# Kernel optimization log

Hardware: AMD Instinct MI355X
Metric: run time of the kernel (lower is better)

The kernel has to match this reference:

```python
import jax, jax.numpy as jnp
import numpy as np


def setup_inputs() -> dict:
    key = jax.random.key(0)
    ks = jax.random.split(key, 5)
    B, C, H, W = 32, 2048, 14, 14
    K = 113  # num_concepts + 1
    NUM_CLASSES = 200
    x = jax.random.normal(ks[0], (B, C, H, W), dtype=jnp.float32)
    concepts = jax.random.normal(ks[1], (K, C), dtype=jnp.float32)
    # small init scale for linear heads (keeps sigmoid/logits in a sane range)
    concept_fc_w = jax.random.normal(ks[2], (1, C), dtype=jnp.float32) * 0.02
    concept_fc_b = jnp.zeros((1,), dtype=jnp.float32)
    label_fc_w = jax.random.normal(ks[3], (NUM_CLASSES, C), dtype=jnp.float32) * 0.02
    label_fc_b = jnp.zeros((NUM_CLASSES,), dtype=jnp.float32)
    return {
        "x": x,
        "concepts": concepts,
        "concept_fc_w": concept_fc_w,
        "concept_fc_b": concept_fc_b,
        "label_fc_w": label_fc_w,
        "label_fc_b": label_fc_b,
    }


def reference(x, concepts, concept_fc_w, concept_fc_b, label_fc_w, label_fc_b):
    b, c, h, w = x.shape
    h2, w2 = h * 2, w * 2
    # F.interpolate(mode='bilinear', align_corners=False) == jax.image.resize bilinear
    x = jax.image.resize(x, (b, c, h2, w2), method="bilinear")
    xe = x.reshape(b, c, h2 * w2).transpose(0, 2, 1)  # [b, n, c]
    # cdist(concepts, xe, p=2) via matmul expansion (matches torch's mm-based cdist)
    x_sq = jnp.sum(xe * xe, axis=-1)                    # [b, n]
    c_sq = jnp.sum(concepts * concepts, axis=-1)        # [k]
    dots = jnp.einsum("kc,bnc->bkn", concepts, xe)      # [b, k, n]
    d2 = c_sq[None, :, None] + x_sq[:, None, :] - 2.0 * dots
    dists = jnp.sqrt(jnp.maximum(d2, 0.0))              # [b, k, n]
    attn = jax.nn.softmax(-dists, axis=1)               # softmax over concepts
    score_maps = attn.reshape(b, -1, h2, w2)            # [b, k, h2, w2]
    concept_vecs = jnp.einsum("bkn,bnc->bkc", attn[:, :-1, :], xe)  # [b, k-1, c]
    logits = jnp.einsum("bkc,c->bk", concept_vecs, concept_fc_w[0]) + concept_fc_b[0]
    concept_scores = jax.nn.sigmoid(logits)             # [b, k-1]
    preds = (concept_scores @ concepts[:-1, :]) @ label_fc_w.T + label_fc_b  # [b, 200]
    return score_maps, concept_scores, preds
```

## Files before the change

kernel.cpp:

```cpp
#include <hip/hip_runtime.h>
#include <hip/hip_bf16.h>
#include <cstdint>

typedef __attribute__((ext_vector_type(8))) short short8;
typedef __attribute__((ext_vector_type(4))) float f32x4;
typedef __attribute__((ext_vector_type(16))) float f32x16;

#define BDIM 32
#define CDIM 2048
#define NPIX 196
#define HIN 14
#define N2 784
#define W2 28
#define KDIM 113
#define KC 112
#define NCLS 200
#define NBX 14
#define BNC 56
#define NSTEP 64
#define PST 224
#define GST 200
#define RDST 68
#define SSTB 60

__global__ __launch_bounds__(256) void k_prep(const float* __restrict__ concepts,
                                              const float* __restrict__ cfcw,
                                              ushort* __restrict__ cbf,
                                              float* __restrict__ csq) {
  int k = blockIdx.x, t = threadIdx.x;
  const int kt = k >> 5, row = k & 31;
  float s = 0.f;
  for (int c = t; c < CDIM; c += 256) {
    float v = (k < KDIM) ? concepts[(size_t)k * CDIM + c] : (k == KDIM ? cfcw[c] : 0.f);
    __hip_bfloat16 h = __float2bfloat16(v);
    int st = c >> 5, it = (c >> 4) & 1, g2 = (c >> 3) & 1, j = c & 7;
    cbf[(((size_t)st * 4 + kt) * 2 + it) * 512 + (g2 * 32 + row) * 8 + j] = __bfloat16_as_ushort(h);
    float vb = __bfloat162float(h);
    s = fmaf(vb, vb, s);
  }
  __shared__ float r[4];
#pragma unroll
  for (int off = 32; off > 0; off >>= 1) s += __shfl_down(s, off, 64);
  if ((t & 63) == 0) r[t >> 6] = s;
  __syncthreads();
  if (t == 0) csq[k] = r[0] + r[1] + r[2] + r[3];
}

__global__ __launch_bounds__(512, 2) void k_xt(const float* __restrict__ x,
                                               ushort* __restrict__ xt,
                                               float* __restrict__ Gpart) {
  __shared__ float P[32 * PST];
  __shared__ float Gw[8][16][65];
  const int sg = blockIdx.x, b = blockIdx.y;
  const int tid = threadIdx.x;
  const int lane = tid & 63, wv = tid >> 6;
  const int chg = tid >> 4, seg = tid & 15;
  const int p0 = seg * 13;

  for (int z = tid; z < 32 * 28; z += 512) {
    int c = z / 28, j = z - c * 28;
    P[c * PST + 196 + j] = 0.f;
  }

  float g[13][5];
#pragma unroll
  for (int p = 0; p < 13; ++p)
#pragma unroll
    for (int t = 0; t < 5; ++t) g[p][t] = 0.f;

  for (int si = 0; si < 4; ++si) {
    const int s = sg * 4 + si;
    __syncthreads();
    {
      const float4* src = (const float4*)(x + ((size_t)b * CDIM + s * 32) * NPIX);
#pragma unroll
      for (int i = 0; i < 3; ++i) {
        int q = tid + i * 512;
        int c = q / 49, pq = q - c * 49;
        *(float4*)&P[c * PST + 4 * pq] = src[q];
      }
      if (tid < 32) {
        int q = 1536 + tid;
        int c = q / 49, pq = q - c * 49;
        *(float4*)&P[c * PST + 4 * pq] = src[q];
      }
    }
    __syncthreads();
#pragma unroll
    for (int pass = 0; pass < 2; ++pass) {
      int slot = tid + pass * 512;
      if (slot < 896) {
        int t = slot >> 7, r = slot & 127;
        int it = r >> 6, l = r & 63;
        int pxp = t * 32 + (l & 31);
        int row = pxp >> 4, col = pxp & 15;
        int c0 = it * 16 + (l >> 5) * 8;
        uint uu[4];
        if (col < 14) {
          int px = row * HIN + col;
#pragma unroll
          for (int p = 0; p < 4; ++p) {
            float v0 = P[(c0 + 2 * p) * PST + px];
            float v1 = P[(c0 + 2 * p + 1) * PST + px];
            uu[p] = (uint)__bfloat16_as_ushort(__float2bfloat16(v0)) |
                    ((uint)__bfloat16_as_ushort(__float2bfloat16(v1)) << 16);
          }
        } else {
          uu[0] = uu[1] = uu[2] = uu[3] = 0u;
        }
        uint4 pk; pk.x = uu[0]; pk.y = uu[1]; pk.z = uu[2]; pk.w = uu[3];
        *(uint4*)&xt[((((size_t)b * 7 + t) * 64 + s) * 1024) + it * 512 + (size_t)l * 8] = pk;
      }
    }
    {
      float xv[28];
      const float* Pr = &P[chg * PST];
#pragma unroll
      for (int i = 0; i < 7; ++i) *(float4*)&xv[4 * i] = *(const float4*)&Pr[p0 + 4 * i];
#pragma unroll
      for (int p = 0; p < 13; ++p) {
        float a = xv[p];
        g[p][0] = fmaf(a, a, g[p][0]);
        g[p][1] = fmaf(a, xv[p + 1], g[p][1]);
        g[p][2] = fmaf(a, xv[p + 13], g[p][2]);
        g[p][3] = fmaf(a, xv[p + 14], g[p][3]);
        g[p][4] = fmaf(a, xv[p + 15], g[p][4]);
      }
    }
  }
#pragma unroll
  for (int p = 0; p < 13; ++p)
#pragma unroll
    for (int t = 0; t < 5; ++t) {
      float v = g[p][t];
      v += __shfl_xor(v, 16, 64);
      v += __shfl_xor(v, 32, 64);
      g[p][t] = v;
    }
  if (lane < 16) {
#pragma unroll
    for (int p = 0; p < 13; ++p)
#pragma unroll
      for (int t = 0; t < 5; ++t) Gw[wv][lane][p * 5 + t] = g[p][t];
  }
  __syncthreads();
#pragma unroll
  for (int it = 0; it < 2; ++it) {
    int slot = tid + it * 512;
    if (slot < 16 * 65) {
      int sseg = slot / 65, i = slot - sseg * 65;
      float v = 0.f;
#pragma unroll
      for (int ww = 0; ww < 8; ++ww) v += Gw[ww][sseg][i];
      int pl = i / 5, ty = i - pl * 5;
      int px = sseg * 13 + pl;
      if (px < NPIX)
        Gpart[((size_t)b * 16 + sg) * (5 * GST) + ty * GST + px] = v;
    }
  }
}

__global__ __launch_bounds__(256) void k_gred(const float* __restrict__ Gpart,
                                              float* __restrict__ Gs) {
  const int b = blockIdx.x, tid = threadIdx.x;
  for (int i = tid; i < 5 * GST; i += 256) {
    float v = 0.f;
#pragma unroll
    for (int sg = 0; sg < 16; ++sg) v += Gpart[((size_t)b * 16 + sg) * (5 * GST) + i];
    Gs[(size_t)b * (5 * GST) + i] = v;
  }
}

__global__ __launch_bounds__(256, 3) void k_gemm3(
    const ushort* __restrict__ xt,
    const ushort* __restrict__ cbf,
    const float* __restrict__ Gs,
    const float* __restrict__ csq,
    float* __restrict__ attn_out,
    float* __restrict__ part)
{
  __shared__ float RDs[128 * RDST];
  __shared__ ushort Ssb[KDIM * SSTB];
  __shared__ float csq_s[KDIM];
  __shared__ float xsqs[BNC], projs2[BNC];

  const int tid = threadIdx.x;
  const int wgid = blockIdx.x;
  const int xcd = wgid & 7, slot = wgid >> 3;
  const int bq = slot / NBX, bx = slot - bq * NBX;
  const int b = xcd + 8 * bq;
  const int n0 = bx * BNC;
  const int lane = tid & 63, w = tid >> 6;

  int r0 = bx - 1; if (r0 < 0) r0 = 0; if (r0 > 11) r0 = 11;
  const int T0 = r0 >> 1;

  if (tid < KDIM) csq_s[tid] = csq[tid];

  const ushort* abp = cbf + w * 1024 + lane * 8;
  const ushort* xtb = xt + (((size_t)b * 7 + T0) << 16) + lane * 8;

  f32x16 acc[2];
#pragma unroll
  for (int tt = 0; tt < 2; ++tt)
#pragma unroll
    for (int r = 0; r < 16; ++r) acc[tt][r] = 0.f;

#define LOADSET(A_, B_, S_)                                              \
  do {                                                                   \
    const size_t so_ = (size_t)(S_) * 4096;                              \
    const size_t xo_ = (size_t)(S_) * 1024;                              \
    A_[0] = *(const uint4*)(abp + so_);                                  \
    A_[1] = *(const uint4*)(abp + so_ + 512);                            \
    B_[0][0] = *(const uint4*)(xtb + xo_);                               \
    B_[0][1] = *(const uint4*)(xtb + xo_ + 512);                         \
    B_[1][0] = *(const uint4*)(xtb + 65536 + xo_);                       \
    B_[1][1] = *(const uint4*)(xtb + 65536 + xo_ + 512);                 \
  } while (0)

#define COMPUTE(A_, B_)                                                  \
  do {                                                                   \
    _Pragma("unroll")                                                    \
    for (int it_ = 0; it_ < 2; ++it_) {                                  \
      short8 af_ = *(const short8*)&A_[it_];                             \
      acc[0] = __builtin_amdgcn_mfma_f32_32x32x16_bf16(                  \
          af_, *(const short8*)&B_[0][it_], acc[0], 0, 0, 0);            \
      acc[1] = __builtin_amdgcn_mfma_f32_32x32x16_bf16(                  \
          af_, *(const short8*)&B_[1][it_], acc[1], 0, 0, 0);            \
    }                                                                    \
  } while (0)

  uint4 a0[2], a1[2], b0[2][2], b1[2][2];
  LOADSET(a0, b0, 0);
  for (int s = 0; s < NSTEP; s += 2) {
    if (s + 1 < NSTEP) LOADSET(a1, b1, s + 1);
    COMPUTE(a0, b0);
    if (s + 2 < NSTEP) LOADSET(a0, b0, s + 2);
    COMPUTE(a1, b1);
  }
#undef LOADSET
#undef COMPUTE

#pragma unroll
  for (int tt = 0; tt < 2; ++tt)
#pragma unroll
    for (int r = 0; r < 16; ++r) {
      int row = w * 32 + (r & 3) + 8 * (r >> 2) + 4 * (lane >> 5);
      RDs[row * RDST + tt * 32 + (lane & 31)] = acc[tt][r];
    }
  __syncthreads();

  auto COLW = [&](int col, int& p1, int& p3, int& p1g, int& p3g,
                  float& w00, float& w01, float& w10, float& w11) {
    const int i2 = 2 * bx + (col >= 28 ? 1 : 0);
    const int j2 = col - (col >= 28 ? 28 : 0);
    float si = 0.5f * i2 - 0.25f, sj = 0.5f * j2 - 0.25f;
    float fif = floorf(si), fjf = floorf(sj);
    int ii = (int)fif, jj = (int)fjf;
    float fi = si - fif, fj = sj - fjf;
    int ia = ii < 0 ? 0 : ii; int ib = (ii + 1 > 13) ? 13 : ii + 1;
    int ja = jj < 0 ? 0 : jj; int jb = (jj + 1 > 13) ? 13 : jj + 1;
    w00 = (1.f - fi) * (1.f - fj); w01 = (1.f - fi) * fj;
    w10 = fi * (1.f - fj);         w11 = fi * fj;
    if (ib == ia) { w00 += w10; w01 += w11; w10 = 0.f; w11 = 0.f; }
    if (jb == ja) { w00 += w01; w10 += w11; w01 = 0.f; w11 = 0.f; }
    p1g = ia * HIN + ja; p3g = ib * HIN + ja;
    p1 = ia * 16 + ja - T0 * 32; p3 = ib * 16 + ja - T0 * 32;
  };

  if (tid < BNC) {
    int p1, p3, p1g, p3g; float w00, w01, w10, w11;
    COLW(tid, p1, p3, p1g, p3g, w00, w01, w10, w11);
    const float* Gb = Gs + (size_t)b * (5 * GST);
    const float* Gd = Gb, *Gr = Gb + GST, *Gy = Gb + 2 * GST, *Gv = Gb + 3 * GST, *Gx = Gb + 4 * GST;
    float xsq = w00 * w00 * Gd[p1g] + w01 * w01 * Gd[p1g + 1]
              + w10 * w10 * Gd[p3g] + w11 * w11 * Gd[p3g + 1]
              + 2.f * (w00 * w01 * Gr[p1g] + w10 * w11 * Gr[p3g]
                     + w00 * w10 * Gv[p1g] + w01 * w11 * Gv[p1g + 1]
                     + w00 * w11 * Gx[p1g] + w01 * w10 * Gy[p1g + 1]);
    const float* rp = &RDs[113 * RDST];
    float pj = w00 * rp[p1] + w01 * rp[p1 + 1] + w10 * rp[p3] + w11 * rp[p3 + 1];
    xsqs[tid] = xsq; projs2[tid] = pj;
  }
  __syncthreads();

  if (tid < BNC * 4) {
    const int col = tid >> 2, sub = tid & 3;
    int p1, p3, p1g, p3g; float w00, w01, w10, w11;
    COLW(col, p1, p3, p1g, p3g, w00, w01, w10, w11);
    const float xq = xsqs[col];
    float ev[29];
    float mx = -1e30f;
#pragma unroll
    for (int i = 0; i < 29; ++i) {
      int k = sub + 4 * i;
      if (k < KDIM) {
        const float* rk = &RDs[k * RDST];
        float dot = w00 * rk[p1] + w01 * rk[p1 + 1] + w10 * rk[p3] + w11 * rk[p3 + 1];
        float d2 = csq_s[k] + xq - 2.f * dot;
        float sv = -sqrtf(fmaxf(d2, 0.f));
        ev[i] = sv;
        mx = fmaxf(mx, sv);
      }
    }
    mx = fmaxf(mx, __shfl_xor(mx, 1, 64));
    mx = fmaxf(mx, __shfl_xor(mx, 2, 64));
    float ssum = 0.f;
#pragma unroll
    for (int i = 0; i < 29; ++i) {
      int k = sub + 4 * i;
      if (k < KDIM) {
        float e = __expf(ev[i] - mx);
        ev[i] = e;
        Ssb[k * SSTB + col] = __bfloat16_as_ushort(__float2bfloat16(e));
        ssum += e;
      }
    }
    ssum += __shfl_xor(ssum, 1, 64);
    ssum += __shfl_xor(ssum, 2, 64);
    const float rinv = 1.f / ssum;
    float* op = attn_out + (size_t)b * KDIM * N2 + n0 + col;
#pragma unroll
    for (int i = 0; i < 29; ++i) {
      int k = sub + 4 * i;
      if (k < KDIM) op[(size_t)k * N2] = ev[i] * rinv;
    }
    if (sub == 0) projs2[col] *= rinv;
  }
  __syncthreads();

  if (tid < KC * 2) {
    const int k = tid >> 1, s2 = tid & 1;
    float lg = 0.f;
    for (int c2 = s2; c2 < BNC; c2 += 2)
      lg = fmaf(__uint_as_float((uint)Ssb[k * SSTB + c2] << 16), projs2[c2], lg);
    lg += __shfl_xor(lg, 1, 64);
    if (s2 == 0) part[((size_t)b * NBX + bx) * KC + k] = lg;
  }
}

__global__ __launch_bounds__(256) void k_tmp(
    const float* __restrict__ concepts, const float* __restrict__ part,
    const float* __restrict__ cfcb, float* __restrict__ cs_out,
    float* __restrict__ tmp) {
  __shared__ float cs_s[KC];
  const int b = blockIdx.y, cx = blockIdx.x;
  const int t = threadIdx.x;
  if (t < KC) {
    float l = cfcb[0];
#pragma unroll
    for (int q = 0; q < NBX; ++q) l += part[((size_t)b * NBX + q) * KC + t];
    float csv = 1.f / (1.f + __expf(-l));
    cs_s[t] = csv;
    if (cx == 0) cs_out[b * KC + t] = csv;
  }
  __syncthreads();
  const int c = cx * 256 + t;
  float a = 0.f;
#pragma unroll 8
  for (int k = 0; k < KC; ++k) a = fmaf(cs_s[k], concepts[(size_t)k * CDIM + c], a);
  tmp[(size_t)b * CDIM + c] = a;
}

__global__ __launch_bounds__(256) void k_pred2(
    const float* __restrict__ labw, const float* __restrict__ labb,
    const float* __restrict__ tmp, float* __restrict__ preds) {
  const int w = blockIdx.x * 4 + (threadIdx.x >> 6);
  const int lane = threadIdx.x & 63;
  const int b = w / NCLS, cls = w % NCLS;
  if (b >= BDIM) return;
  const float* tr = tmp + (size_t)b * CDIM;
  const float* wr = labw + (size_t)cls * CDIM;
  float a = 0.f;
#pragma unroll
  for (int c0 = 0; c0 < CDIM; c0 += 256) {
    float4 t = *(const float4*)&tr[c0 + lane * 4];
    float4 v = *(const float4*)&wr[c0 + lane * 4];
    a += t.x * v.x + t.y * v.y + t.z * v.z + t.w * v.w;
  }
#pragma unroll
  for (int off = 32; off > 0; off >>= 1) a += __shfl_down(a, off, 64);
  if (lane == 0) preds[b * NCLS + cls] = a + labb[cls];
}

extern "C" void kernel_launch(void* const* d_in, const int* in_sizes, int n_in,
                              void* d_out, int out_size, void* d_ws, size_t ws_size,
                              hipStream_t stream) {
  const float* x        = (const float*)d_in[0];
  const float* concepts = (const float*)d_in[1];
  const float* cfcw     = (const float*)d_in[2];
  const float* cfcb     = (const float*)d_in[3];
  const float* labw     = (const float*)d_in[4];
  const float* labb     = (const float*)d_in[5];

  float* out    = (float*)d_out;
  float* sm_out = out;
  float* cs_out = out + (size_t)BDIM * KDIM * N2;
  float* pr_out = cs_out + (size_t)BDIM * KC;

  char* ws = (char*)d_ws;
  float*  csq   = (float*)(ws + 0);
  float*  part  = (float*)(ws + 512);
  ushort* cbf   = (ushort*)(ws + 201216);
  float*  tmp   = (float*)(ws + 725504);
  float*  Gpart = (float*)(ws + 987648);
  float*  Gs    = (float*)(ws + 3035648);
  ushort* xt    = (ushort*)(ws + 3163648);

  k_prep <<<dim3(128), dim3(256), 0, stream>>>(concepts, cfcw, cbf, csq);
  k_xt   <<<dim3(16, BDIM), dim3(512), 0, stream>>>(x, xt, Gpart);
  k_gred <<<dim3(BDIM), dim3(256), 0, stream>>>(Gpart, Gs);
  k_gemm3<<<dim3(448), dim3(256), 0, stream>>>(xt, cbf, Gs, csq, sm_out, part);
  k_tmp  <<<dim3(CDIM / 256, BDIM), dim3(256), 0, stream>>>(concepts, part, cfcb, cs_out, tmp);
  k_pred2<<<dim3((BDIM * NCLS + 3) / 4), dim3(256), 0, stream>>>(labw, labb, tmp, pr_out);
}
```

Before: 90.42 us.

## Double-buffer x tiles in k_xt with register prefetch and reuse LDS for reduction

k_xt now prefetches the next 32-channel slab of x into registers while it processes the current one out of a second LDS buffer. This overlaps global load latency with the transpose and Gram computation, and drops one barrier per iteration. The reduction scratch Gw now aliases the P buffer, which keeps LDS use modest, and launch bounds are raised to request 4 blocks per CU. The trade-off is higher register pressure from the prefetched float4s and the 65 g accumulators under the tighter launch bound, which could cause spills.

```diff
diff --git a/kernel.cpp b/kernel.cpp
--- a/kernel.cpp
+++ b/kernel.cpp
@@ -46,20 +46,25 @@
   if (t == 0) csq[k] = r[0] + r[1] + r[2] + r[3];
 }
 
-__global__ __launch_bounds__(512, 2) void k_xt(const float* __restrict__ x,
+__global__ __launch_bounds__(512, 4) void k_xt(const float* __restrict__ x,
                                                ushort* __restrict__ xt,
                                                float* __restrict__ Gpart) {
-  __shared__ float P[32 * PST];
-  __shared__ float Gw[8][16][65];
+  __shared__ float P[2][32 * PST];
   const int sg = blockIdx.x, b = blockIdx.y;
   const int tid = threadIdx.x;
   const int lane = tid & 63, wv = tid >> 6;
   const int chg = tid >> 4, seg = tid & 15;
   const int p0 = seg * 13;
 
-  for (int z = tid; z < 32 * 28; z += 512) {
-    int c = z / 28, j = z - c * 28;
-    P[c * PST + 196 + j] = 0.f;
+  const int c0a = tid / 49,           pq0 = tid - c0a * 49;
+  const int c1a = (tid + 512) / 49,   pq1 = (tid + 512) - c1a * 49;
+  const int c2a = (tid + 1024) / 49,  pq2 = (tid + 1024) - c2a * 49;
+  const int c3a = (tid + 1536) / 49,  pq3 = (tid + 1536) - c3a * 49;
+
+  for (int z = tid; z < 2 * 32 * 28; z += 512) {
+    int buf = z / 896, r = z - buf * 896;
+    int c = r / 28, j = r - c * 28;
+    P[buf][c * PST + 196 + j] = 0.f;
   }
 
   float g[13][5];
@@ -67,25 +72,29 @@
   for (int p = 0; p < 13; ++p)
 #pragma unroll
     for (int t = 0; t < 5; ++t) g[p][t] = 0.f;
+
+  float4 q0, q1, q2, q3 = {0.f, 0.f, 0.f, 0.f};
+  auto LOADQ = [&](int s) {
+    const float4* src = (const float4*)(x + ((size_t)b * CDIM + s * 32) * NPIX);
+    q0 = src[tid]; q1 = src[tid + 512]; q2 = src[tid + 1024];
+    if (tid < 32) q3 = src[tid + 1536];
+  };
+  auto WRITEQ = [&](int buf) {
+    float* Pb = P[buf];
+    *(float4*)&Pb[c0a * PST + 4 * pq0] = q0;
+    *(float4*)&Pb[c1a * PST + 4 * pq1] = q1;
+    *(float4*)&Pb[c2a * PST + 4 * pq2] = q2;
+    if (tid < 32) *(float4*)&Pb[c3a * PST + 4 * pq3] = q3;
+  };
+
+  LOADQ(sg * 4);
+  WRITEQ(0);
+  __syncthreads();
 
   for (int si = 0; si < 4; ++si) {
     const int s = sg * 4 + si;
-    __syncthreads();
-    {
-      const float4* src = (const float4*)(x + ((size_t)b * CDIM + s * 32) * NPIX);
-#pragma unroll
-      for (int i = 0; i < 3; ++i) {
-        int q = tid + i * 512;
-        int c = q / 49, pq = q - c * 49;
-        *(float4*)&P[c * PST + 4 * pq] = src[q];
-      }
-      if (tid < 32) {
-        int q = 1536 + tid;
-        int c = q / 49, pq = q - c * 49;
-        *(float4*)&P[c * PST + 4 * pq] = src[q];
-      }
-    }
-    __syncthreads();
+    const int cur = si & 1;
+    if (si < 3) LOADQ(s + 1);
 #pragma unroll
     for (int pass = 0; pass < 2; ++pass) {
       int slot = tid + pass * 512;
@@ -100,8 +109,8 @@
           int px = row * HIN + col;
 #pragma unroll
           for (int p = 0; p < 4; ++p) {
-            float v0 = P[(c0 + 2 * p) * PST + px];
-            float v1 = P[(c0 + 2 * p + 1) * PST + px];
+            float v0 = P[cur][(c0 + 2 * p) * PST + px];
+            float v1 = P[cur][(c0 + 2 * p + 1) * PST + px];
             uu[p] = (uint)__bfloat16_as_ushort(__float2bfloat16(v0)) |
                     ((uint)__bfloat16_as_ushort(__float2bfloat16(v1)) << 16);
           }
@@ -114,7 +123,7 @@
     }
     {
       float xv[28];
-      const float* Pr = &P[chg * PST];
+      const float* Pr = &P[cur][chg * PST];
 #pragma unroll
       for (int i = 0; i < 7; ++i) *(float4*)&xv[4 * i] = *(const float4*)&Pr[p0 + 4 * i];
 #pragma unroll
@@ -127,7 +136,11 @@
         g[p][4] = fmaf(a, xv[p + 15], g[p][4]);
       }
     }
-  }
+    if (si < 3) WRITEQ((si + 1) & 1);
+    __syncthreads();
+  }
+
+  float* Gw = &P[0][0];
 #pragma unroll
   for (int p = 0; p < 13; ++p)
 #pragma unroll
@@ -141,7 +154,7 @@
 #pragma unroll
     for (int p = 0; p < 13; ++p)
 #pragma unroll
-      for (int t = 0; t < 5; ++t) Gw[wv][lane][p * 5 + t] = g[p][t];
+      for (int t = 0; t < 5; ++t) Gw[((size_t)wv * 16 + lane) * 65 + p * 5 + t] = g[p][t];
   }
   __syncthreads();
 #pragma unroll
@@ -151,7 +164,7 @@
       int sseg = slot / 65, i = slot - sseg * 65;
       float v = 0.f;
 #pragma unroll
-      for (int ww = 0; ww < 8; ++ww) v += Gw[ww][sseg][i];
+      for (int ww = 0; ww < 8; ++ww) v += Gw[((size_t)ww * 16 + sseg) * 65 + i];
       int pl = i / 5, ty = i - pl * 5;
       int px = sseg * 13 + pl;
       if (px < NPIX)
```

New measurement: 84.64 us (median of 2 runs). 1.07x faster.
